# Kernel tuning notes

Hardware: AMD Instinct MI355X
Metric: run time of the kernel (lower is better)

Reference implementation:

```python
import jax, jax.numpy as jnp
import numpy as np

THRESHOLD = 0.5
EPS_STD = 1e-08
EPS_DEG = 1e-08


def setup_inputs() -> dict:
    key = jax.random.key(0)
    x = jax.random.normal(key, (32, 64, 1000, 16), dtype=jnp.float32)
    return {"x": x}


def reference(x):
    # x: [B, C, T, F]
    B, C, T, F = x.shape
    # permute(0,1,3,2).reshape(B, C, F*T)
    xr = jnp.transpose(x, (0, 1, 3, 2)).reshape(B, C, F * T)
    mean = jnp.mean(xr, axis=2, keepdims=True)
    # torch.std is unbiased (ddof=1)
    std = jnp.std(xr, axis=2, keepdims=True, ddof=1) + EPS_STD
    xn = (xr - mean) / std
    # [B, C, C] correlation-style adjacency (note: divided by T, as in source)
    adj = jnp.einsum('bcd,bed->bce', xn, xn) / T
    adj = (adj > THRESHOLD).astype(x.dtype)
    adj = adj + jnp.eye(C, dtype=x.dtype)[None, :, :]
    degree = jnp.sum(adj, axis=2, keepdims=True)            # [B, C, 1]
    dsi = (degree + EPS_DEG) ** -0.5
    adj = adj * dsi * jnp.transpose(dsi, (0, 2, 1))          # D^-1/2 A D^-1/2
    return adj
```

## Files before the change

### kernel.cpp

```cpp
#include <hip/hip_runtime.h>

#define B_SZ 32
#define C_CH 64
#define D_TOT 16000
#define NP 25
#define CHUNK 640
#define KT 128
#define NT 5

typedef short bf16x8 __attribute__((ext_vector_type(8)));
typedef float f32x4 __attribute__((ext_vector_type(4)));

#define PARTG_ELEMS (NP * B_SZ * 4096)
#define PARTS_ELEMS (NP * B_SZ * 64)

__device__ __forceinline__ unsigned f2bf_pk(float a, float b) {
    unsigned ua = __builtin_bit_cast(unsigned, a);
    unsigned ub = __builtin_bit_cast(unsigned, b);
    ua = (ua + 0x7FFFu + ((ua >> 16) & 1u)) >> 16;
    ub = (ub + 0x7FFFu + ((ub >> 16) & 1u)) >> 16;
    return (ua & 0xFFFFu) | (ub << 16);
}

__global__ __launch_bounds__(256) void gram_mfma(
    const float* __restrict__ x, float* __restrict__ partG, float* __restrict__ partS)
{
    __shared__ __align__(16) short tile[2][C_CH * KT];

    const int t = threadIdx.x;
    const int b = blockIdx.y;
    const int chunk = blockIdx.x;
    const int l = t & 63;
    const int w = t >> 6;
    const int w0 = (w >> 1) * 32;
    const int w1 = (w & 1) * 32;

    const float* xb = x + (size_t)b * (C_CH * D_TOT) + chunk * CHUNK;

    const int lch = t >> 5;
    const int ldp = (t & 31) * 4;
    const float* rp[8];
    int wb[8];
    #pragma unroll
    for (int j = 0; j < 8; ++j) {
        const int ch = lch + 8 * j;
        rp[j] = xb + (size_t)ch * D_TOT + ldp;
        wb[j] = (ch * 256 + ldp * 2) ^ ((ch & 7) << 4);
    }

    const int fl = l & 15;
    const int fg = (l >> 4) * 16;

    f32x4 acc[2][2];
    #pragma unroll
    for (int i = 0; i < 2; ++i)
        #pragma unroll
        for (int k = 0; k < 2; ++k)
            acc[i][k] = (f32x4){0.f, 0.f, 0.f, 0.f};

    float ssum[8];
    #pragma unroll
    for (int j = 0; j < 8; ++j) ssum[j] = 0.f;

    float4 ld[8];

#define CVT_STORE(BUFIDX)                                                        \
    {                                                                            \
        char* buf_ = (char*)tile[BUFIDX];                                        \
        _Pragma("unroll")                                                        \
        for (int j = 0; j < 8; ++j) {                                            \
            const float4 v = ld[j];                                              \
            ssum[j] += v.x + v.y + v.z + v.w;                                    \
            uint2 u;                                                             \
            u.x = f2bf_pk(v.x, v.y);                                             \
            u.y = f2bf_pk(v.z, v.w);                                             \
            *reinterpret_cast<uint2*>(buf_ + wb[j]) = u;                         \
        }                                                                        \
    }

    #pragma unroll
    for (int j = 0; j < 8; ++j) ld[j] = *reinterpret_cast<const float4*>(rp[j]);
    CVT_STORE(0)
    #pragma unroll
    for (int j = 0; j < 8; ++j) ld[j] = *reinterpret_cast<const float4*>(rp[j] + KT);
    __syncthreads();

    #pragma unroll
    for (int tt = 0; tt < NT; ++tt) {
        if (tt + 1 < NT) {
            CVT_STORE((tt + 1) & 1)
            if (tt + 2 < NT) {
                #pragma unroll
                for (int j = 0; j < 8; ++j)
                    ld[j] = *reinterpret_cast<const float4*>(rp[j] + (tt + 2) * KT);
            }
        }
        {
            const char* buf = (const char*)tile[tt & 1];
            #pragma unroll
            for (int kk = 0; kk < 4; ++kk) {
                const int k64 = kk * 64;
                const int chA0 = w0 + fl,      chA1 = w0 + 16 + fl;
                const int chB0 = w1 + fl,      chB1 = w1 + 16 + fl;
                const bf16x8 a0 = *reinterpret_cast<const bf16x8*>(
                    buf + ((chA0 * 256 + fg + k64) ^ ((chA0 & 7) << 4)));
                const bf16x8 a1 = *reinterpret_cast<const bf16x8*>(
                    buf + ((chA1 * 256 + fg + k64) ^ ((chA1 & 7) << 4)));
                const bf16x8 b0 = *reinterpret_cast<const bf16x8*>(
                    buf + ((chB0 * 256 + fg + k64) ^ ((chB0 & 7) << 4)));
                const bf16x8 b1 = *reinterpret_cast<const bf16x8*>(
                    buf + ((chB1 * 256 + fg + k64) ^ ((chB1 & 7) << 4)));
                acc[0][0] = __builtin_amdgcn_mfma_f32_16x16x32_bf16(a0, b0, acc[0][0], 0, 0, 0);
                acc[0][1] = __builtin_amdgcn_mfma_f32_16x16x32_bf16(a0, b1, acc[0][1], 0, 0, 0);
                acc[1][0] = __builtin_amdgcn_mfma_f32_16x16x32_bf16(a1, b0, acc[1][0], 0, 0, 0);
                acc[1][1] = __builtin_amdgcn_mfma_f32_16x16x32_bf16(a1, b1, acc[1][1], 0, 0, 0);
            }
        }
        __syncthreads();
    }
#undef CVT_STORE

    const size_t pbase = (size_t)(chunk * B_SZ + b);
    #pragma unroll
    for (int j = 0; j < 8; ++j) {
        float v = ssum[j];
        v += __shfl_xor(v, 1);
        v += __shfl_xor(v, 2);
        v += __shfl_xor(v, 4);
        v += __shfl_xor(v, 8);
        v += __shfl_xor(v, 16);
        if ((t & 31) == 0) partS[pbase * 64 + lch + 8 * j] = v;
    }

    float* gOut = partG + pbase * 4096;
    const int crow = w0 + ((l >> 4) << 2);
    const int ccol = w1 + fl;
    #pragma unroll
    for (int ct = 0; ct < 2; ++ct)
        #pragma unroll
        for (int tj = 0; tj < 2; ++tj)
            #pragma unroll
            for (int r = 0; r < 4; ++r)
                gOut[(crow + ct * 16 + r) * 64 + (ccol + tj * 16)] = acc[ct][tj][r];
}

__global__ __launch_bounds__(256) void reduce_g(
    const float* __restrict__ partG, float* __restrict__ redG)
{
    const int i = blockIdx.x * 256 + threadIdx.x;
    const int b = i >> 10;
    const int o = (i & 1023) * 4;
    f32x4 s = (f32x4){0.f, 0.f, 0.f, 0.f};
    #pragma unroll
    for (int c = 0; c < NP; ++c)
        s += *reinterpret_cast<const f32x4*>(partG + ((size_t)(c * B_SZ + b)) * 4096 + o);
    *reinterpret_cast<f32x4*>(redG + (size_t)b * 4096 + o) = s;
}

__global__ __launch_bounds__(256) void finalize_kernel(
    const float* __restrict__ redG, const float* __restrict__ partS, float* __restrict__ out)
{
    __shared__ float shS[64];
    __shared__ float shStd[64];
    __shared__ float shDeg[64];
    __shared__ float shDsi[64];
    __shared__ float shBin[64][65];
    const int b = blockIdx.x;
    const int t = threadIdx.x;
    const float* G = redG + (size_t)b * 4096;

    if (t < 64) {
        float S = 0.f;
        #pragma unroll
        for (int c = 0; c < NP; ++c)
            S += partS[(size_t)(c * B_SZ + b) * 64 + t];
        const float gcc = G[t * 64 + t];
        const float mean = S * (1.0f / 16000.0f);
        const float var = (gcc - S * mean) * (1.0f / 15999.0f);
        shS[t] = S;
        shStd[t] = sqrtf(var) + 1e-8f;
    }
    __syncthreads();

    const int r  = t >> 2;
    const int cb = (t & 3) * 16;
    const float Sc = shS[r];
    const float stdc = shStd[r];
    float deg = 0.0f;
    #pragma unroll
    for (int m = 0; m < 16; ++m) {
        const int e = cb + m;
        const float g = G[r * 64 + e];
        const float a = (g - Sc * shS[e] * (1.0f / 16000.0f)) / (stdc * shStd[e] * 1000.0f);
        float bin = (a > 0.5f) ? 1.0f : 0.0f;
        if (e == r) bin += 1.0f;
        shBin[r][e] = bin;
        deg += bin;
    }
    deg += __shfl_xor(deg, 1);
    deg += __shfl_xor(deg, 2);
    if ((t & 3) == 0) shDeg[r] = deg;
    __syncthreads();
    if (t < 64) shDsi[t] = 1.0f / sqrtf(shDeg[t] + 1e-8f);
    __syncthreads();

    float* ob = out + (size_t)b * 4096;
    const float dr = shDsi[r];
    #pragma unroll
    for (int m = 0; m < 16; ++m) {
        const int e = cb + m;
        ob[r * 64 + e] = shBin[r][e] * dr * shDsi[e];
    }
}

extern "C" void kernel_launch(void* const* d_in, const int* in_sizes, int n_in,
                              void* d_out, int out_size, void* d_ws, size_t ws_size,
                              hipStream_t stream)
{
    const float* x = (const float*)d_in[0];
    float* out = (float*)d_out;
    float* partG = (float*)d_ws;
    float* partS = partG + PARTG_ELEMS;
    float* redG  = partS + PARTS_ELEMS;

    gram_mfma<<<dim3(NP, B_SZ), 256, 0, stream>>>(x, partG, partS);
    reduce_g<<<128, 256, 0, stream>>>(partG, redG);
    finalize_kernel<<<B_SZ, 256, 0, stream>>>(redG, partS, out);
}
```

Measured before the change: 198.2 us.

## Use fewer longer split-K chunks with deeper two-set register prefetch

Cuts the split-K partition count from 25 to 8, so each block now walks 15-16 KT tiles instead of 5, which shrinks the partial Gram buffers and the reduction work. The main loop becomes a runtime loop with two register load sets, keeping two tiles of global loads in flight while one tile is converted and another is computed from LDS. In exchange the grid drops to 256 blocks, lowering parallelism on a many-CU GPU, and the larger live register set may reduce occupancy.

```diff
diff --git a/kernel.cpp b/kernel.cpp
--- a/kernel.cpp
+++ b/kernel.cpp
@@ -3,10 +3,8 @@
 #define B_SZ 32
 #define C_CH 64
 #define D_TOT 16000
-#define NP 25
-#define CHUNK 640
+#define NP 8
 #define KT 128
-#define NT 5
 
 typedef short bf16x8 __attribute__((ext_vector_type(8)));
 typedef float f32x4 __attribute__((ext_vector_type(4)));
@@ -30,12 +28,15 @@
     const int t = threadIdx.x;
     const int b = blockIdx.y;
     const int chunk = blockIdx.x;
+    const int nt = (chunk < 5) ? 16 : 15;
+    const int t0 = (chunk < 5) ? chunk * 16 : 80 + (chunk - 5) * 15;
+
     const int l = t & 63;
     const int w = t >> 6;
     const int w0 = (w >> 1) * 32;
     const int w1 = (w & 1) * 32;
 
-    const float* xb = x + (size_t)b * (C_CH * D_TOT) + chunk * CHUNK;
+    const float* xb = x + (size_t)b * (C_CH * D_TOT) + t0 * KT;
 
     const int lch = t >> 5;
     const int ldp = (t & 31) * 4;
@@ -62,14 +63,21 @@
     #pragma unroll
     for (int j = 0; j < 8; ++j) ssum[j] = 0.f;
 
-    float4 ld[8];
-
-#define CVT_STORE(BUFIDX)                                                        \
+    float4 ldA[8], ldB[8];
+
+#define ISSUE(SET, TI)                                                           \
+    {                                                                            \
+        _Pragma("unroll")                                                        \
+        for (int j = 0; j < 8; ++j)                                              \
+            SET[j] = *reinterpret_cast<const float4*>(rp[j] + (TI) * KT);        \
+    }
+
+#define CVT_STORE(SET, BUFIDX)                                                   \
     {                                                                            \
         char* buf_ = (char*)tile[BUFIDX];                                        \
         _Pragma("unroll")                                                        \
         for (int j = 0; j < 8; ++j) {                                            \
-            const float4 v = ld[j];                                              \
+            const float4 v = SET[j];                                             \
             ssum[j] += v.x + v.y + v.z + v.w;                                    \
             uint2 u;                                                             \
             u.x = f2bf_pk(v.x, v.y);                                             \
@@ -78,47 +86,55 @@
         }                                                                        \
     }
 
-    #pragma unroll
-    for (int j = 0; j < 8; ++j) ld[j] = *reinterpret_cast<const float4*>(rp[j]);
-    CVT_STORE(0)
-    #pragma unroll
-    for (int j = 0; j < 8; ++j) ld[j] = *reinterpret_cast<const float4*>(rp[j] + KT);
-    __syncthreads();
-
-    #pragma unroll
-    for (int tt = 0; tt < NT; ++tt) {
-        if (tt + 1 < NT) {
-            CVT_STORE((tt + 1) & 1)
-            if (tt + 2 < NT) {
-                #pragma unroll
-                for (int j = 0; j < 8; ++j)
-                    ld[j] = *reinterpret_cast<const float4*>(rp[j] + (tt + 2) * KT);
+#define COMPUTE(BUFIDX)                                                          \
+    {                                                                            \
+        const char* buf = (const char*)tile[BUFIDX];                             \
+        _Pragma("unroll")                                                        \
+        for (int kk = 0; kk < 4; ++kk) {                                         \
+            const int k64 = kk * 64;                                             \
+            const int chA0 = w0 + fl,      chA1 = w0 + 16 + fl;                  \
+            const int chB0 = w1 + fl,      chB1 = w1 + 16 + fl;                  \
+            const bf16x8 a0 = *reinterpret_cast<const bf16x8*>(                  \
+                buf + ((chA0 * 256 + fg + k64) ^ ((chA0 & 7) << 4)));            \
+            const bf16x8 a1 = *reinterpret_cast<const bf16x8*>(                  \
+                buf + ((chA1 * 256 + fg + k64) ^ ((chA1 & 7) << 4)));            \
+            const bf16x8 b0 = *reinterpret_cast<const bf16x8*>(                  \
+                buf + ((chB0 * 256 + fg + k64) ^ ((chB0 & 7) << 4)));            \
+            const bf16x8 b1 = *reinterpret_cast<const bf16x8*>(                  \
+                buf + ((chB1 * 256 + fg + k64) ^ ((chB1 & 7) << 4)));            \
+            acc[0][0] = __builtin_amdgcn_mfma_f32_16x16x32_bf16(a0, b0, acc[0][0], 0, 0, 0); \
+            acc[0][1] = __builtin_amdgcn_mfma_f32_16x16x32_bf16(a0, b1, acc[0][1], 0, 0, 0); \
+            acc[1][0] = __builtin_amdgcn_mfma_f32_16x16x32_bf16(a1, b0, acc[1][0], 0, 0, 0); \
+            acc[1][1] = __builtin_amdgcn_mfma_f32_16x16x32_bf16(a1, b1, acc[1][1], 0, 0, 0); \
+        }                                                                        \
+    }
+
+    ISSUE(ldA, 0)
+    ISSUE(ldB, 1)
+    CVT_STORE(ldA, 0)
+    ISSUE(ldA, 2)
+    __syncthreads();
+
+    for (int tt = 0; tt < nt; tt += 2) {
+        if (tt + 1 < nt) {
+            CVT_STORE(ldB, 1)
+            if (tt + 3 < nt) ISSUE(ldB, tt + 3)
+        }
+        COMPUTE(0)
+        __syncthreads();
+
+        if (tt + 1 < nt) {
+            if (tt + 2 < nt) {
+                CVT_STORE(ldA, 0)
+                if (tt + 4 < nt) ISSUE(ldA, tt + 4)
             }
+            COMPUTE(1)
+            __syncthreads();
         }
-        {
-            const char* buf = (const char*)tile[tt & 1];
-            #pragma unroll
-            for (int kk = 0; kk < 4; ++kk) {
-                const int k64 = kk * 64;
-                const int chA0 = w0 + fl,      chA1 = w0 + 16 + fl;
-                const int chB0 = w1 + fl,      chB1 = w1 + 16 + fl;
-                const bf16x8 a0 = *reinterpret_cast<const bf16x8*>(
-                    buf + ((chA0 * 256 + fg + k64) ^ ((chA0 & 7) << 4)));
-                const bf16x8 a1 = *reinterpret_cast<const bf16x8*>(
-                    buf + ((chA1 * 256 + fg + k64) ^ ((chA1 & 7) << 4)));
-                const bf16x8 b0 = *reinterpret_cast<const bf16x8*>(
-                    buf + ((chB0 * 256 + fg + k64) ^ ((chB0 & 7) << 4)));
-                const bf16x8 b1 = *reinterpret_cast<const bf16x8*>(
-                    buf + ((chB1 * 256 + fg + k64) ^ ((chB1 & 7) << 4)));
-                acc[0][0] = __builtin_amdgcn_mfma_f32_16x16x32_bf16(a0, b0, acc[0][0], 0, 0, 0);
-                acc[0][1] = __builtin_amdgcn_mfma_f32_16x16x32_bf16(a0, b1, acc[0][1], 0, 0, 0);
-                acc[1][0] = __builtin_amdgcn_mfma_f32_16x16x32_bf16(a1, b0, acc[1][0], 0, 0, 0);
-                acc[1][1] = __builtin_amdgcn_mfma_f32_16x16x32_bf16(a1, b1, acc[1][1], 0, 0, 0);
-            }
-        }
-        __syncthreads();
-    }
+    }
+#undef ISSUE
 #undef CVT_STORE
+#undef COMPUTE
 
     const size_t pbase = (size_t)(chunk * B_SZ + b);
     #pragma unroll
```

Result: no change. 197.3 us (-0.5%).
